# Kernel tuning notes

Measured on AMD Instinct MI355X. Metric: run time of the kernel, lower is better.

Reference implementation:

```python
import jax, jax.numpy as jnp
import numpy as np

NUM_EMBEDDINGS = 1024
EMBEDDING_DIM = 256
BETA = 0.25


def setup_inputs() -> dict:
    key = jax.random.key(0)
    k1, k2 = jax.random.split(key)
    x = jax.random.normal(k1, (32, 256, 32, 32), dtype=jnp.float32)
    # nn.Embedding weight init: uniform(-1/K, 1/K)
    lim = 1.0 / NUM_EMBEDDINGS
    emb_weight = jax.random.uniform(k2, (NUM_EMBEDDINGS, EMBEDDING_DIM),
                                    dtype=jnp.float32, minval=-lim, maxval=lim)
    return {"x": x, "emb_weight": emb_weight}


def reference(x, emb_weight):
    b, c, h, w = x.shape
    # [b, h, w, c] -> [N, c]
    x_flat = jnp.transpose(x, (0, 2, 3, 1)).reshape(-1, c)
    distances = (jnp.sum(x_flat * x_flat, axis=1, keepdims=True)
                 - 2.0 * jnp.einsum('nc,kc->nk', x_flat, emb_weight)
                 + jnp.sum(emb_weight * emb_weight, axis=1))
    indices = jnp.argmin(distances, axis=1)  # [N]
    quantized = emb_weight[indices].reshape(b, h, w, c).transpose(0, 3, 1, 2)
    sg = jax.lax.stop_gradient
    commitment_loss = jnp.mean((sg(quantized) - x) ** 2)
    embedding_loss = jnp.mean((quantized - sg(x)) ** 2)
    loss = commitment_loss + BETA * embedding_loss
    return quantized, loss, indices.reshape(b, h, w)
```

## Files before the change

### kernel.cpp

```cpp
#include <hip/hip_runtime.h>

#define LOSS_OFF 8388608
#define IDX_OFF  8388609

#define WS_SEE   0
#define WS_SXX   4096
#define WS_KEY   135168
#define WS_CNT   397312
#define WS_LOSS  397320
#define WS_WL    397328
#define WS_EP    528448

#define FLT_BIG  3.402823466e+38f
#define MARGIN   1.0e-4f

typedef __attribute__((ext_vector_type(8))) short  short8v;
typedef __attribute__((ext_vector_type(4))) float  float4v;

__device__ __forceinline__ float np_sumsq256(const float* __restrict__ p, int stride) {
    float s[2];
#pragma unroll
    for (int half = 0; half < 2; half++) {
        const float* a = p + half * 128 * stride;
        float r[8];
#pragma unroll
        for (int l = 0; l < 8; l++) {
            float v = a[l * stride];
            float sq = v * v;
            asm volatile("" : "+v"(sq));
            r[l] = sq;
        }
#pragma unroll
        for (int i = 8; i < 128; i += 8) {
#pragma unroll
            for (int l = 0; l < 8; l++) {
                float v = a[(i + l) * stride];
                float sq = v * v;
                asm volatile("" : "+v"(sq));
                r[l] = r[l] + sq;
            }
        }
        s[half] = ((r[0] + r[1]) + (r[2] + r[3])) + ((r[4] + r[5]) + (r[6] + r[7]));
    }
    return s[0] + s[1];
}

__device__ __forceinline__ unsigned int f32_sortable(float m) {
    unsigned int u = __float_as_uint(m);
    return u ^ (((unsigned int)((int)u >> 31)) | 0x80000000u);
}

__device__ __forceinline__ unsigned short f2bf(float f) {
    unsigned int u = __float_as_uint(f);
    return (unsigned short)((u + 0x7fffu + ((u >> 16) & 1u)) >> 16);
}
__device__ __forceinline__ float bf2f(unsigned short h) {
    return __uint_as_float(((unsigned int)h) << 16);
}

__global__ __launch_bounds__(256) void k0_see(const float* __restrict__ emb,
                                              float* __restrict__ see,
                                              int* __restrict__ cnt,
                                              double* __restrict__ loss) {
    const int k = blockIdx.x * 256 + threadIdx.x;
    see[k] = np_sumsq256(emb + (size_t)k * 256, 1);
    if (k == 0) { *cnt = 0; *loss = 0.0; }
}

__global__ __launch_bounds__(256) void k_epack(const float* __restrict__ emb,
                                               unsigned short* __restrict__ ebP) {
    const int idx = blockIdx.x * 256 + threadIdx.x;
    const int l  = idx & 63;
    const int ph = (idx >> 6) & 1;
    const int ct = (idx >> 7) & 7;
    const int cc = (idx >> 10) & 7;
    const int cg = (idx >> 13) & 7;
    const int row = cg * 128 + ct * 16 + (l & 15);
    const int col = cc * 32 + (l >> 4) * 8;
    const float* src = emb + (size_t)row * 256 + col;
    uint4 out;
    unsigned short* op = (unsigned short*)&out;
#pragma unroll
    for (int i = 0; i < 8; i++) {
        const float v = src[i];
        const unsigned short h = f2bf(v);
        op[i] = ph ? f2bf(v - bf2f(h)) : h;
    }
    *(uint4*)(ebP + (size_t)idx * 8) = out;
}

__global__ __launch_bounds__(256) void k_et(const float* __restrict__ emb,
                                            float* __restrict__ eT) {
    __shared__ float T[256][17];
    const int t  = threadIdx.x;
    const int k0 = blockIdx.x << 4;
    const int kr = t >> 4, cs = (t & 15) << 4;
#pragma unroll
    for (int j = 0; j < 4; j++) {
        const float4 v = *(const float4*)(emb + (size_t)(k0 + kr) * 256 + cs + j * 4);
        T[cs + j * 4 + 0][kr] = v.x;
        T[cs + j * 4 + 1][kr] = v.y;
        T[cs + j * 4 + 2][kr] = v.z;
        T[cs + j * 4 + 3][kr] = v.w;
    }
    __syncthreads();
    float* dst = eT + (size_t)t * 1024 + k0;
#pragma unroll
    for (int j = 0; j < 4; j++) {
        float4 v;
        v.x = T[t][j * 4 + 0]; v.y = T[t][j * 4 + 1];
        v.z = T[t][j * 4 + 2]; v.w = T[t][j * 4 + 3];
        *(float4*)(dst + j * 4) = v;
    }
}

__global__ __launch_bounds__(256) void k_xpack(const float* __restrict__ x,
                                               unsigned short* __restrict__ axP,
                                               float* __restrict__ sxx) {
    __shared__ float xs[256 * 33];
    const int t = threadIdx.x, rs = blockIdx.x;
    const int row = t & 31, cg = t >> 5;
    const int b = rs >> 5;
    const int hw0 = (rs & 31) << 5;
    const float* xb = x + (size_t)b * 262144 + hw0 + row;
#pragma unroll 4
    for (int cc2 = 0; cc2 < 32; cc2++) {
        const int c = cg * 32 + cc2;
        xs[c * 33 + row] = xb[(size_t)c * 1024];
    }
    __syncthreads();
#pragma unroll
    for (int ii = 0; ii < 4; ii++) {
        const int ci = ii * 256 + t;
        const int l = ci & 63;
        const int rowg = (ci >> 6) & 1;
        const int cc = ci >> 7;
        const int r = rowg * 16 + (l & 15);
        const int c0 = cc * 32 + (l >> 4) * 8;
        uint4 hp, lp;
        unsigned short* hpp = (unsigned short*)&hp;
        unsigned short* lpp = (unsigned short*)&lp;
#pragma unroll
        for (int i = 0; i < 8; i++) {
            const float v = xs[(c0 + i) * 33 + r];
            const unsigned short h = f2bf(v);
            hpp[i] = h;
            lpp[i] = f2bf(v - bf2f(h));
        }
        const size_t base = ((size_t)rs * 8 + cc) * 2 + rowg;
        *(uint4*)(axP + ((base * 2 + 0) * 64 + l) * 8) = hp;
        *(uint4*)(axP + ((base * 2 + 1) * 64 + l) * 8) = lp;
    }
    if (t < 32) sxx[rs * 32 + t] = np_sumsq256(xs + t, 33);
}

__global__ __launch_bounds__(512, 2) void k1_mfma(
        const unsigned short* __restrict__ axP,
        const unsigned short* __restrict__ ebP,
        const float* __restrict__ see_g,
        unsigned long long* __restrict__ key,
        int* __restrict__ cnt, int* __restrict__ wl) {
    __shared__ unsigned long long lk1[64][8];
    __shared__ float lg1[64][8];
    __shared__ float lg2[64][8];
    const int t = threadIdx.x;
    const int codeg = t >> 6, l = t & 63;
    const int lrow = l >> 4, lcol = l & 15;
    const int rb = blockIdx.x;
    const int n0 = rb * 64;

    float4v acc[4][8];
#pragma unroll
    for (int at = 0; at < 4; at++)
#pragma unroll
        for (int ct = 0; ct < 8; ct++) acc[at][ct] = (float4v){0.f, 0.f, 0.f, 0.f};

#pragma unroll
    for (int cc = 0; cc < 8; cc++) {
        short8v ah[4], al[4];
#pragma unroll
        for (int at = 0; at < 4; at++) {
            const size_t ab = ((((size_t)(rb * 2 + (at >> 1)) * 8 + cc) * 2 + (at & 1)) * 2)
                              * 512 + (size_t)l * 8;
            ah[at] = *(const short8v*)(axP + ab);
            al[at] = *(const short8v*)(axP + ab + 512);
        }
#pragma unroll
        for (int ct = 0; ct < 8; ct++) {
            const size_t bb = ((((size_t)codeg * 8 + cc) * 8 + ct) * 2) * 512 + (size_t)l * 8;
            const short8v bh = *(const short8v*)(ebP + bb);
            const short8v bl = *(const short8v*)(ebP + bb + 512);
#pragma unroll
            for (int at = 0; at < 4; at++) {
                acc[at][ct] = __builtin_amdgcn_mfma_f32_16x16x32_bf16(ah[at], bh, acc[at][ct], 0, 0, 0);
                acc[at][ct] = __builtin_amdgcn_mfma_f32_16x16x32_bf16(ah[at], bl, acc[at][ct], 0, 0, 0);
                acc[at][ct] = __builtin_amdgcn_mfma_f32_16x16x32_bf16(al[at], bh, acc[at][ct], 0, 0, 0);
            }
        }
    }

    float sv[8];
#pragma unroll
    for (int ct = 0; ct < 8; ct++) sv[ct] = see_g[codeg * 128 + ct * 16 + lcol];

#pragma unroll
    for (int at = 0; at < 4; at++) {
#pragma unroll
        for (int j = 0; j < 4; j++) {
            unsigned long long K1 = ~0ull; float G1 = FLT_BIG, G2 = FLT_BIG;
#pragma unroll
            for (int ct = 0; ct < 8; ct++) {
                const float g = fmaf(-2.f, acc[at][ct][j], sv[ct]);
                const int k = codeg * 128 + ct * 16 + lcol;
                const unsigned long long pk =
                    ((unsigned long long)f32_sortable(g) << 32) | (unsigned int)k;
                if (pk < K1) { G2 = G1; K1 = pk; G1 = g; }
                else         { G2 = fminf(G2, g); }
            }
#pragma unroll
            for (int m = 1; m < 16; m <<= 1) {
                const unsigned long long oK = __shfl_xor(K1, m, 64);
                const float oG1 = __shfl_xor(G1, m, 64);
                const float oG2 = __shfl_xor(G2, m, 64);
                if (oK < K1) { G2 = fminf(oG2, G1); K1 = oK; G1 = oG1; }
                else         { G2 = fminf(G2, oG1); }
            }
            const int rloc = at * 16 + lrow * 4 + j;
            if (lcol == 0) { lk1[rloc][codeg] = K1; lg1[rloc][codeg] = G1; lg2[rloc][codeg] = G2; }
        }
    }
    __syncthreads();
    if (t < 64) {
        unsigned long long K1 = ~0ull; float G1 = FLT_BIG, G2 = FLT_BIG;
        for (int cg = 0; cg < 8; cg++) {
            const unsigned long long oK = lk1[t][cg];
            const float oG1 = lg1[t][cg], oG2 = lg2[t][cg];
            if (oK < K1) { G2 = fminf(oG2, G1); K1 = oK; G1 = oG1; }
            else         { G2 = fminf(G2, oG1); }
        }
        const int n = n0 + t;
        if (G2 - G1 > MARGIN) { key[n] = K1; }
        else { key[n] = ~0ull; wl[atomicAdd(cnt, 1)] = n; }
    }
}

__global__ __launch_bounds__(256) void k2r(const float* __restrict__ x,
                                           const float* __restrict__ eT,
                                           const float* __restrict__ see,
                                           const float* __restrict__ sxx,
                                           unsigned long long* __restrict__ key,
                                           const int* __restrict__ cnt,
                                           const int* __restrict__ wl) {
    __shared__ float xs[8][264];
    const int t = threadIdx.x;
    const int total = *cnt;
    for (int base = blockIdx.x * 8; base < total; base += 128 * 8) {
        int nrow[8]; float sx8[8];
#pragma unroll
        for (int r = 0; r < 8; r++) {
            int idx = base + r; if (idx >= total) idx = total - 1;
            const int n = wl[idx];
            nrow[r] = n; sx8[r] = sxx[n];
        }
        __syncthreads();
#pragma unroll
        for (int r = 0; r < 8; r++) {
            const int n = nrow[r];
            xs[r][t] = x[(size_t)(n >> 10) * 262144 + (size_t)t * 1024 + (n & 1023)];
        }
        __syncthreads();
        float d[8][4];
#pragma unroll
        for (int r = 0; r < 8; r++)
#pragma unroll
            for (int j = 0; j < 4; j++) d[r][j] = 0.f;
#pragma unroll 4
        for (int c = 0; c < 256; c++) {
            float ev[4];
#pragma unroll
            for (int j = 0; j < 4; j++) ev[j] = eT[(size_t)c * 1024 + t + 256 * j];
#pragma unroll
            for (int r = 0; r < 8; r++) {
                const float xv = xs[r][c];
                d[r][0] = fmaf(xv, ev[0], d[r][0]);
                d[r][1] = fmaf(xv, ev[1], d[r][1]);
                d[r][2] = fmaf(xv, ev[2], d[r][2]);
                d[r][3] = fmaf(xv, ev[3], d[r][3]);
            }
        }
#pragma unroll
        for (int r = 0; r < 8; r++) {
            unsigned long long best = ~0ull;
#pragma unroll
            for (int j = 0; j < 4; j++) {
                const float q = fmaf(-2.f, d[r][j], sx8[r]) + see[t + 256 * j];
                const unsigned long long pk =
                    ((unsigned long long)f32_sortable(q) << 32) | (unsigned int)(t + 256 * j);
                best = pk < best ? pk : best;
            }
            atomicMin(&key[nrow[r]], best);
        }
    }
}

__global__ __launch_bounds__(256) void k3_out(const float* __restrict__ x,
                                              const float* __restrict__ emb,
                                              const unsigned long long* __restrict__ key,
                                              float* __restrict__ dout,
                                              double* __restrict__ loss) {
    __shared__ float elds[32][257];
    __shared__ int   idxs[32];
    __shared__ float red[256];
    const int t  = threadIdx.x;
    const int bh = blockIdx.x;
    const int b = bh >> 5, h = bh & 31;
    if (t < 32) idxs[t] = (int)(key[(bh << 5) + t] & 0xffffffffull);
    __syncthreads();
    for (int r = 0; r < 32; r++) elds[r][t] = emb[(size_t)idxs[r] * 256 + t];
    __syncthreads();
    const int w = t & 31, cg = t >> 5;
    const size_t base = (size_t)b * 262144 + (size_t)(h * 32 + w);
    float acc = 0.f;
#pragma unroll 4
    for (int s = 0; s < 32; s++) {
        const int c = (cg << 5) + s;
        const float q  = elds[w][c];
        const float xv = x[base + (size_t)c * 1024];
        dout[base + (size_t)c * 1024] = q;
        const float d = q - xv;
        acc = fmaf(d, d, acc);
    }
    red[t] = acc;
    __syncthreads();
    for (int s = 128; s > 0; s >>= 1) {
        if (t < s) red[t] += red[t + s];
        __syncthreads();
    }
    if (t == 0) atomicAdd(loss, (double)red[0]);
    if (t < 32) dout[IDX_OFF + (bh << 5) + t] = (float)idxs[t];
}

__global__ void k4_fin(const double* __restrict__ loss, float* __restrict__ dout) {
    dout[LOSS_OFF] = (float)(1.25 * (*loss) / 8388608.0);
}

extern "C" void kernel_launch(void* const* d_in, const int* in_sizes, int n_in,
                              void* d_out, int out_size, void* d_ws, size_t ws_size,
                              hipStream_t stream) {
    const float* x   = (const float*)d_in[0];
    const float* emb = (const float*)d_in[1];
    float* dout = (float*)d_out;
    char* ws = (char*)d_ws;
    float*  see  = (float*)(ws + WS_SEE);
    float*  sxx  = (float*)(ws + WS_SXX);
    unsigned long long* key = (unsigned long long*)(ws + WS_KEY);
    int*    cnt  = (int*)(ws + WS_CNT);
    double* loss = (double*)(ws + WS_LOSS);
    int*    wl   = (int*)(ws + WS_WL);
    unsigned short* ebP = (unsigned short*)(ws + WS_EP);
    float*  eT   = (float*)(ws + WS_EP);
    unsigned short* axP = (unsigned short*)d_out;

    k0_see <<<4,    256, 0, stream>>>(emb, see, cnt, loss);
    k_epack<<<256,  256, 0, stream>>>(emb, ebP);
    k_xpack<<<1024, 256, 0, stream>>>(x, axP, sxx);
    k1_mfma<<<512,  512, 0, stream>>>(axP, ebP, see, key, cnt, wl);
    k_et   <<<64,   256, 0, stream>>>(emb, eT);
    k2r    <<<128,  256, 0, stream>>>(x, eT, see, sxx, key, cnt, wl);
    k3_out <<<1024, 256, 0, stream>>>(x, emb, key, dout, loss);
    k4_fin <<<1,      1, 0, stream>>>(loss, dout);
}
```

Measured before the change: 205.0 us.

## Stage A tiles in LDS via global_load_lds, merge prep kernels, trim shuffles

```diff
diff --git a/kernel.cpp b/kernel.cpp
--- a/kernel.cpp
+++ b/kernel.cpp
@@ -17,6 +17,10 @@
 typedef __attribute__((ext_vector_type(8))) short  short8v;
 typedef __attribute__((ext_vector_type(4))) float  float4v;
 
+#define GLD16(gp, lp) __builtin_amdgcn_global_load_lds( \
+    (const __attribute__((address_space(1))) unsigned int*)(gp), \
+    (__attribute__((address_space(3))) unsigned int*)(lp), 16, 0, 0)
+
 __device__ __forceinline__ float np_sumsq256(const float* __restrict__ p, int stride) {
     float s[2];
 #pragma unroll
@@ -49,6 +53,10 @@
     unsigned int u = __float_as_uint(m);
     return u ^ (((unsigned int)((int)u >> 31)) | 0x80000000u);
 }
+__device__ __forceinline__ float f32_unsortable(unsigned int s) {
+    const unsigned int u = (s >> 31) ? (s ^ 0x80000000u) : ~s;
+    return __uint_as_float(u);
+}
 
 __device__ __forceinline__ unsigned short f2bf(float f) {
     unsigned int u = __float_as_uint(f);
@@ -58,35 +66,36 @@
     return __uint_as_float(((unsigned int)h) << 16);
 }
 
-__global__ __launch_bounds__(256) void k0_see(const float* __restrict__ emb,
+__global__ __launch_bounds__(256) void k_prep(const float* __restrict__ emb,
+                                              unsigned short* __restrict__ ebP,
                                               float* __restrict__ see,
                                               int* __restrict__ cnt,
                                               double* __restrict__ loss) {
-    const int k = blockIdx.x * 256 + threadIdx.x;
-    see[k] = np_sumsq256(emb + (size_t)k * 256, 1);
-    if (k == 0) { *cnt = 0; *loss = 0.0; }
-}
-
-__global__ __launch_bounds__(256) void k_epack(const float* __restrict__ emb,
-                                               unsigned short* __restrict__ ebP) {
-    const int idx = blockIdx.x * 256 + threadIdx.x;
-    const int l  = idx & 63;
-    const int ph = (idx >> 6) & 1;
-    const int ct = (idx >> 7) & 7;
-    const int cc = (idx >> 10) & 7;
-    const int cg = (idx >> 13) & 7;
-    const int row = cg * 128 + ct * 16 + (l & 15);
-    const int col = cc * 32 + (l >> 4) * 8;
-    const float* src = emb + (size_t)row * 256 + col;
-    uint4 out;
-    unsigned short* op = (unsigned short*)&out;
-#pragma unroll
-    for (int i = 0; i < 8; i++) {
-        const float v = src[i];
-        const unsigned short h = f2bf(v);
-        op[i] = ph ? f2bf(v - bf2f(h)) : h;
-    }
-    *(uint4*)(ebP + (size_t)idx * 8) = out;
+    const int t = threadIdx.x, bb = blockIdx.x;
+    if (bb < 256) {
+        const int idx = bb * 256 + t;
+        const int l  = idx & 63;
+        const int ph = (idx >> 6) & 1;
+        const int ct = (idx >> 7) & 7;
+        const int cc = (idx >> 10) & 7;
+        const int cg = (idx >> 13) & 7;
+        const int row = cg * 128 + ct * 16 + (l & 15);
+        const int col = cc * 32 + (l >> 4) * 8;
+        const float* src = emb + (size_t)row * 256 + col;
+        uint4 out;
+        unsigned short* op = (unsigned short*)&out;
+#pragma unroll
+        for (int i = 0; i < 8; i++) {
+            const float v = src[i];
+            const unsigned short h = f2bf(v);
+            op[i] = ph ? f2bf(v - bf2f(h)) : h;
+        }
+        *(uint4*)(ebP + (size_t)idx * 8) = out;
+    } else {
+        const int k = (bb - 256) * 256 + t;
+        see[k] = np_sumsq256(emb + (size_t)k * 256, 1);
+        if (k == 0) { *cnt = 0; *loss = 0.0; }
+    }
 }
 
 __global__ __launch_bounds__(256) void k_et(const float* __restrict__ emb,
@@ -160,14 +169,16 @@
         const float* __restrict__ see_g,
         unsigned long long* __restrict__ key,
         int* __restrict__ cnt, int* __restrict__ wl) {
-    __shared__ unsigned long long lk1[64][8];
-    __shared__ float lg1[64][8];
-    __shared__ float lg2[64][8];
+    __shared__ char smem[8192];
+    unsigned long long* lk1 = (unsigned long long*)smem;
+    float*              lg2 = (float*)(smem + 4096);
     const int t = threadIdx.x;
     const int codeg = t >> 6, l = t & 63;
     const int lrow = l >> 4, lcol = l & 15;
     const int rb = blockIdx.x;
     const int n0 = rb * 64;
+    const char* aBase = (const char*)axP;
+    char* aDst = smem + codeg * 1024;
 
     float4v acc[4][8];
 #pragma unroll
@@ -175,15 +186,21 @@
 #pragma unroll
         for (int ct = 0; ct < 8; ct++) acc[at][ct] = (float4v){0.f, 0.f, 0.f, 0.f};
 
-#pragma unroll
     for (int cc = 0; cc < 8; cc++) {
+        __syncthreads();
+        {
+            const int sub = codeg >> 2;
+            const char* src = aBase + ((size_t)((rb * 2 + sub) * 8 + cc)) * 4096
+                              + (size_t)(codeg & 3) * 1024 + (size_t)l * 16;
+            GLD16(src, aDst);
+        }
+        __syncthreads();
         short8v ah[4], al[4];
 #pragma unroll
         for (int at = 0; at < 4; at++) {
-            const size_t ab = ((((size_t)(rb * 2 + (at >> 1)) * 8 + cc) * 2 + (at & 1)) * 2)
-                              * 512 + (size_t)l * 8;
-            ah[at] = *(const short8v*)(axP + ab);
-            al[at] = *(const short8v*)(axP + ab + 512);
+            const int off = (at >> 1) * 4096 + (at & 1) * 2048;
+            ah[at] = *(const short8v*)(smem + off + l * 16);
+            al[at] = *(const short8v*)(smem + off + 1024 + l * 16);
         }
 #pragma unroll
         for (int ct = 0; ct < 8; ct++) {
@@ -198,6 +215,7 @@
             }
         }
     }
+    __syncthreads();
 
     float sv[8];
 #pragma unroll
@@ -220,21 +238,22 @@
 #pragma unroll
             for (int m = 1; m < 16; m <<= 1) {
                 const unsigned long long oK = __shfl_xor(K1, m, 64);
-                const float oG1 = __shfl_xor(G1, m, 64);
                 const float oG2 = __shfl_xor(G2, m, 64);
+                const float oG1 = f32_unsortable((unsigned int)(oK >> 32));
                 if (oK < K1) { G2 = fminf(oG2, G1); K1 = oK; G1 = oG1; }
                 else         { G2 = fminf(G2, oG1); }
             }
             const int rloc = at * 16 + lrow * 4 + j;
-            if (lcol == 0) { lk1[rloc][codeg] = K1; lg1[rloc][codeg] = G1; lg2[rloc][codeg] = G2; }
+            if (lcol == 0) { lk1[rloc * 8 + codeg] = K1; lg2[rloc * 8 + codeg] = G2; }
         }
     }
     __syncthreads();
     if (t < 64) {
         unsigned long long K1 = ~0ull; float G1 = FLT_BIG, G2 = FLT_BIG;
         for (int cg = 0; cg < 8; cg++) {
-            const unsigned long long oK = lk1[t][cg];
-            const float oG1 = lg1[t][cg], oG2 = lg2[t][cg];
+            const unsigned long long oK = lk1[t * 8 + cg];
+            const float oG2 = lg2[t * 8 + cg];
+            const float oG1 = f32_unsortable((unsigned int)(oK >> 32));
             if (oK < K1) { G2 = fminf(oG2, G1); K1 = oK; G1 = oG1; }
             else         { G2 = fminf(G2, oG1); }
         }
@@ -361,8 +380,7 @@
     float*  eT   = (float*)(ws + WS_EP);
     unsigned short* axP = (unsigned short*)d_out;
 
-    k0_see <<<4,    256, 0, stream>>>(emb, see, cnt, loss);
-    k_epack<<<256,  256, 0, stream>>>(emb, ebP);
+    k_prep <<<260,  256, 0, stream>>>(emb, ebP, see, cnt, loss);
     k_xpack<<<1024, 256, 0, stream>>>(x, axP, sxx);
     k1_mfma<<<512,  512, 0, stream>>>(axP, ebP, see, key, cnt, wl);
     k_et   <<<64,   256, 0, stream>>>(emb, eT);
```

Result: no change. 204.6 us (-0.2%).
